# Performance work log

Hardware: AMD Instinct MI355X
Metric: run time of the kernel (lower is better)

## Reference

```python
import jax, jax.numpy as jnp
import numpy as np

E = 1024   # embd_size
H = 16     # heads_num
DH = E // H
DFF = 4 * E
B, T = 2, 2048


def layer_norm(x, g, b, eps=1e-5):
    mu = jnp.mean(x, axis=-1, keepdims=True)
    var = jnp.var(x, axis=-1, keepdims=True)
    return (x - mu) * jax.lax.rsqrt(var + eps) * g + b


def setup_inputs() -> dict:
    key = jax.random.key(0)
    ks = jax.random.split(key, 12)
    s = 0.02
    return {
        "x": jax.random.normal(ks[0], (B, T, E), dtype=jnp.float32),
        "Wq": jax.random.normal(ks[1], (E, E), dtype=jnp.float32) * s,
        "Wk": jax.random.normal(ks[2], (E, E), dtype=jnp.float32) * s,
        "Wv": jax.random.normal(ks[3], (E, E), dtype=jnp.float32) * s,
        "Wo": jax.random.normal(ks[4], (E, E), dtype=jnp.float32) * s,
        "bo": jnp.zeros((E,), dtype=jnp.float32),
        "W1": jax.random.normal(ks[5], (E, DFF), dtype=jnp.float32) * s,
        "b1": jnp.zeros((DFF,), dtype=jnp.float32),
        "W2": jax.random.normal(ks[6], (DFF, E), dtype=jnp.float32) * s,
        "b2": jnp.zeros((E,), dtype=jnp.float32),
        "g1": jnp.ones((E,), dtype=jnp.float32),
        "be1": jnp.zeros((E,), dtype=jnp.float32),
        "g2": jnp.ones((E,), dtype=jnp.float32),
        "be2": jnp.zeros((E,), dtype=jnp.float32),
    }


def reference(x, Wq, Wk, Wv, Wo, bo, W1, b1, W2, b2, g1, be1, g2, be2):
    Bx, Tx, C = x.shape
    # --- self-attention sublayer ---
    h = layer_norm(x, g1, be1)
    # per-head projections; heads concatenated along output dim == stacked weights
    q = (h @ Wq).reshape(Bx, Tx, H, DH)  # [B,T,H,Dh]
    k = (h @ Wk).reshape(Bx, Tx, H, DH)
    v = (h @ Wv).reshape(Bx, Tx, H, DH)
    # NOTE: original scales by full embd_size**-0.5 (C = x.shape[-1]), not head_size
    scale = C ** (-0.5)
    scores = jnp.einsum("bqhd,bkhd->bhqk", q, k) * scale  # [B,H,T,T]
    mask = jnp.tril(jnp.ones((Tx, Tx), dtype=bool))
    scores = jnp.where(mask, scores, -jnp.inf)
    attn = jax.nn.softmax(scores, axis=-1)
    o = jnp.einsum("bhqk,bkhd->bqhd", attn, v).reshape(Bx, Tx, C)
    sa = o @ Wo + bo
    x = x + sa
    # --- feed-forward sublayer ---
    h2 = layer_norm(x, g2, be2)
    ff = jax.nn.relu(h2 @ W1 + b1) @ W2 + b2
    return x + ff
```

## Files before the change

kernel.cpp:

```cpp
#include <hip/hip_runtime.h>
#include <hip/hip_bf16.h>
#include <math.h>

#define Bn 2
#define Tn 2048
#define En 1024
#define Hn 16
#define DFFn 4096
#define Mn (Bn*Tn)
#define QKVLD 3072

typedef __hip_bfloat16 bf16;
typedef unsigned short u16;
typedef unsigned int u32;
typedef __attribute__((ext_vector_type(8))) short short8;
typedef __attribute__((ext_vector_type(4))) float f32x4;

typedef __attribute__((address_space(1))) const void cg_void;
typedef __attribute__((address_space(3))) void lds_void;

#define QSC 0.0450842200278f

#define HBAR() asm volatile("s_waitcnt lgkmcnt(0)\n\ts_barrier" ::: "memory")

__device__ __forceinline__ u16 f2bf(float f) {
    bf16 h = __float2bfloat16(f);
    u16 u; __builtin_memcpy(&u, &h, 2); return u;
}
__device__ __forceinline__ float bf2f(u16 u) {
    u32 x = ((u32)u) << 16; float f; __builtin_memcpy(&f, &x, 4); return f;
}

__global__ __launch_bounds__(256)
void transpose_w4(const float* __restrict__ s0, const float* __restrict__ s1,
                  const float* __restrict__ s2, const float* __restrict__ s3,
                  u16* __restrict__ d0, u16* __restrict__ d1,
                  u16* __restrict__ d2, u16* __restrict__ d3) {
    const float* src = (blockIdx.z == 0) ? s0 : (blockIdx.z == 1) ? s1
                     : (blockIdx.z == 2) ? s2 : s3;
    u16* dst = (blockIdx.z == 0) ? d0 : (blockIdx.z == 1) ? d1
             : (blockIdx.z == 2) ? d2 : d3;
    __shared__ float t[64][65];
    const int r0 = blockIdx.y * 64, c0 = blockIdx.x * 64;
    const int tr = threadIdx.x >> 6, tc = threadIdx.x & 63;
#pragma unroll
    for (int i = 0; i < 16; i++)
        t[tr + i * 4][tc] = src[(size_t)(r0 + tr + i * 4) * 1024 + c0 + tc];
    __syncthreads();
#pragma unroll
    for (int i = 0; i < 16; i++)
        dst[(size_t)(c0 + tr + i * 4) * 1024 + r0 + tc] = f2bf(t[tc][tr + i * 4]);
}

__global__ __launch_bounds__(256)
void transpose_w(const float* __restrict__ src, u16* __restrict__ dst,
                 int R, int C) {
    __shared__ float t[64][65];
    const int r0 = blockIdx.y * 64, c0 = blockIdx.x * 64;
    const int tr = threadIdx.x >> 6, tc = threadIdx.x & 63;
#pragma unroll
    for (int i = 0; i < 16; i++)
        t[tr + i * 4][tc] = src[(size_t)(r0 + tr + i * 4) * C + c0 + tc];
    __syncthreads();
#pragma unroll
    for (int i = 0; i < 16; i++)
        dst[(size_t)(c0 + tr + i * 4) * R + r0 + tc] = f2bf(t[tc][tr + i * 4]);
}

__global__ __launch_bounds__(256)
void vcopy_t(const u16* __restrict__ QKV, u16* __restrict__ Vg) {
    const int bh = blockIdx.z;
    const int t0 = blockIdx.y * 64;
    __shared__ u16 t[64][65];
    const int tr = threadIdx.x >> 6, tc = threadIdx.x & 63;
    const u16* src = QKV + (size_t)(bh >> 4) * 2048 * QKVLD + 2048 + (bh & 15) * 64;
#pragma unroll
    for (int i = 0; i < 16; i++)
        t[tr + i * 4][tc] = src[(size_t)(t0 + tr + i * 4) * QKVLD + tc];
    __syncthreads();
    u16* dst = Vg + (size_t)bh * 64 * 2048;
#pragma unroll
    for (int i = 0; i < 16; i++)
        dst[(size_t)(tr + i * 4) * 2048 + t0 + tc] = t[tc][tr + i * 4];
}

template<typename AT>
__global__ __launch_bounds__(256)
void ln_kernel(const AT* __restrict__ x, const float* __restrict__ g,
               const float* __restrict__ b, u16* __restrict__ out) {
    const int row = blockIdx.x;
    const int tid = threadIdx.x;
    const AT* xp = x + (size_t)row * En;
    float v[4];
    float s = 0.f, sq = 0.f;
#pragma unroll
    for (int i = 0; i < 4; i++) {
        if constexpr (sizeof(AT) == 2) v[i] = bf2f(xp[tid + i * 256]);
        else                           v[i] = (float)xp[tid + i * 256];
        s += v[i];
        sq += v[i] * v[i];
    }
    __shared__ float rs[256], rq[256];
    rs[tid] = s; rq[tid] = sq;
    __syncthreads();
    for (int st = 128; st > 0; st >>= 1) {
        if (tid < st) { rs[tid] += rs[tid + st]; rq[tid] += rq[tid + st]; }
        __syncthreads();
    }
    const float mu  = rs[0] * (1.0f / En);
    const float var = rq[0] * (1.0f / En) - mu * mu;
    const float inv = rsqrtf(var + 1e-5f);
#pragma unroll
    for (int i = 0; i < 4; i++) {
        const int c = tid + i * 256;
        out[(size_t)row * En + c] = f2bf((v[i] - mu) * inv * g[c] + b[c]);
    }
}

__global__ __launch_bounds__(256)
void ff2_init(const u16* __restrict__ X1, const float* __restrict__ b2,
              float* __restrict__ out) {
    const int row = blockIdx.x;
    const int c = threadIdx.x * 4;
    ushort4 a = *(const ushort4*)&X1[(size_t)row * En + c];
    float4 bb = *(const float4*)&b2[c];
    float4 o;
    o.x = bf2f(a.x) + bb.x;
    o.y = bf2f(a.y) + bb.y;
    o.z = bf2f(a.z) + bb.z;
    o.w = bf2f(a.w) + bb.w;
    *(float4*)&out[(size_t)row * En + c] = o;
}

template<int TM, int HAS_BIAS, int RELU, int RES, int OUT_F32, int SCQ,
         int SPLITC, int SPLITA, int ATOM = 0, int XSWZ = 0>
__global__ __launch_bounds__(256)
void gemm_bt(const u16* __restrict__ A, const u16* __restrict__ A2, int ldA,
             const u16* __restrict__ Wt, int ldW,
             const float* __restrict__ bias, const void* __restrict__ res,
             void* __restrict__ Cout, void* __restrict__ Cout2,
             int ldC, int Kd) {
    constexpr int IF = TM / 32;
    __shared__ __align__(16) u16 As[TM * 32];
    __shared__ __align__(16) u16 Bs[128 * 32];
    const int tid  = threadIdx.x;
    const int lane = tid & 63, wv = tid >> 6;
    const int quad = lane >> 4, l16 = lane & 15;

    int bx = blockIdx.x, by = blockIdx.y, bz = blockIdx.z;
    if (XSWZ) {
        const int GX = gridDim.x, GY = gridDim.y;
        const int L = (bz * GY + by) * GX + bx;
        const int xcd = L & 7, slot = L >> 3;
        const int p = slot / GX;
        bx = slot - p * GX;
        const int yz = p * 8 + xcd;
        by = yz & (GY - 1);
        bz = yz >> __builtin_ctz(GY);
    }

    const int m0 = by * TM, n0 = bx * 128;
    const int rw = (wv >> 1) * (TM / 2), cw = (wv & 1) * 64;
    const int lr  = lane >> 2;
    const int gsw = ((lane & 3) ^ ((lane >> 3) & 3)) * 8;
    const int psw = (quad ^ ((l16 >> 1) & 3)) * 8;

    f32x4 acc[IF][4] = {};

    const int kbase = ATOM ? bz * Kd : 0;
    for (int kt = kbase; kt < kbase + Kd; kt += 32) {
        const u16* Ap = (SPLITA && kt >= 2048) ? A2 : A;
        const int  kk = SPLITA ? (kt & 2047) : kt;
        __syncthreads();
#pragma unroll
        for (int t = 0; t < TM / 64; t++) {
            const int row = wv * (TM / 4) + t * 16;
            __builtin_amdgcn_global_load_lds(
                (cg_void*)(const void*)&Ap[(size_t)(m0 + row + lr) * ldA + kk + gsw],
                (lds_void*)(void*)&As[row * 32], 16, 0, 0);
        }
#pragma unroll
        for (int t = 0; t < 2; t++) {
            const int row = wv * 32 + t * 16;
            __builtin_amdgcn_global_load_lds(
                (cg_void*)(const void*)&Wt[(size_t)(n0 + row + lr) * ldW + kt + gsw],
                (lds_void*)(void*)&Bs[row * 32], 16, 0, 0);
        }
        __syncthreads();

        short8 af[IF], bfr[4];
#pragma unroll
        for (int i = 0; i < IF; i++)
            af[i] = *(const short8*)&As[(rw + i * 16 + l16) * 32 + psw];
#pragma unroll
        for (int j = 0; j < 4; j++)
            bfr[j] = *(const short8*)&Bs[(cw + j * 16 + l16) * 32 + psw];
#pragma unroll
        for (int i = 0; i < IF; i++)
#pragma unroll
            for (int j = 0; j < 4; j++)
                acc[i][j] = __builtin_amdgcn_mfma_f32_16x16x32_bf16(
                    af[i], bfr[j], acc[i][j], 0, 0, 0);
    }

    const float qscale = (SCQ && n0 < 1024) ? QSC : 1.0f;
    void* Cp = (SPLITC && n0 >= 2048) ? Cout2 : Cout;
#pragma unroll
    for (int i = 0; i < IF; i++) {
#pragma unroll
        for (int r = 0; r < 4; r++) {
            const int gm = m0 + rw + i * 16 + quad * 4 + r;
#pragma unroll
            for (int j = 0; j < 4; j++) {
                const int gn = n0 + cw + j * 16 + l16;
                const int cn = SPLITC ? (gn & 2047) : gn;
                float c = acc[i][j][r];
                if (HAS_BIAS) c += bias[gn];
                if (RELU) c = fmaxf(c, 0.f);
                if (RES == 1) c += ((const float*)res)[(size_t)gm * ldC + cn];
                if (RES == 2) c += bf2f(((const u16*)res)[(size_t)gm * ldC + cn]);
                if (SCQ) c *= qscale;
                if (ATOM) {
                    atomicAdd(&((float*)Cp)[(size_t)gm * ldC + cn], c);
                } else if (OUT_F32) {
                    ((float*)Cp)[(size_t)gm * ldC + cn] = c;
                } else {
                    ((u16*)Cp)[(size_t)gm * ldC + cn] = f2bf(c);
                }
            }
        }
    }
}

__global__ __launch_bounds__(256)
void flash_pass1(const u16* __restrict__ QKV, const u16* __restrict__ Vg,
                 u16* __restrict__ Op0, u16* __restrict__ Op1qkv,
                 float* __restrict__ stats) {
    const int pr = blockIdx.x >> 1, half = blockIdx.x & 1;
    const int hh = blockIdx.y, bb = blockIdx.z;
    const int tid  = threadIdx.x;
    const int lane = tid & 63, wv = tid >> 6;
    const int quad = lane >> 4, l16 = lane & 15;

    __shared__ __align__(16) u16 Ks[2][64 * 64];
    __shared__ __align__(16) u16 Vt[2][64 * 64];
    __shared__ __align__(16) u16 Ps[4][16 * 64];

    const size_t rowbase = (size_t)(bb * Tn) * QKVLD;
    const u16* Vgh = Vg + (size_t)(bb * Hn + hh) * 64 * 2048;

    const int sr = tid >> 2;
    const int p0 = (tid & 3) | ((sr & 1) << 2);
    const int p1 = p0 ^ 4;
    const int g0 = p0 ^ (sr & 7), g1 = p1 ^ (sr & 7);
    const int lsw = l16 & 7;

    uint4 kA, kB, vA, vB;
    auto prefetch = [&](int kt) {
        const size_t kb = rowbase + (size_t)(kt * 64 + sr) * QKVLD + 1024 + hh * 64;
        kA = *(const uint4*)&QKV[kb + g0 * 8];
        kB = *(const uint4*)&QKV[kb + g1 * 8];
        const size_t vb = (size_t)sr * 2048 + kt * 64;
        vA = *(const uint4*)&Vgh[vb + g0 * 8];
        vB = *(const uint4*)&Vgh[vb + g1 * 8];
    };
    auto writebuf = [&](int buf) {
        *(uint4*)&Ks[buf][sr * 64 + p0 * 8] = kA;
        *(uint4*)&Ks[buf][sr * 64 + p1 * 8] = kB;
        *(uint4*)&Vt[buf][sr * 64 + p0 * 8] = vA;
        *(uint4*)&Vt[buf][sr * 64 + p1 * 8] = vB;
    };

    for (int qsel = 0; qsel < 2; qsel++) {
        const int qt = qsel ? (31 - pr) : pr;
        const int nk = (qt >= half) ? ((qt - half) >> 1) + 1 : 0;
        const int qrow = qt * 64 + wv * 16 + l16;
        const int grow = bb * Tn + qrow;

        f32x4 ot[4] = {};
        float m2 = -INFINITY, lrow = 0.f;

        HBAR();
        if (nk > 0) {
            const u16* qp = QKV + rowbase + (size_t)qrow * QKVLD + hh * 64;
            short8 qf[2];
            qf[0] = *(const short8*)&qp[quad * 8];
            qf[1] = *(const short8*)&qp[32 + quad * 8];

            prefetch(half);
            writebuf(0);
            if (nk > 1) prefetch(half + 2);
            HBAR();

            const bool hasdiag = ((qt ^ half) & 1) == 0;
            for (int f = 0; f < nk; f++) {
                const int cur = f & 1;

                f32x4 st[4] = {};
#pragma unroll
                for (int ks = 0; ks < 2; ks++)
#pragma unroll
                    for (int i = 0; i < 4; i++) {
                        short8 kf = *(const short8*)&Ks[cur][(i * 16 + l16) * 64 +
                                     (((ks * 4 + quad) ^ lsw) * 8)];
                        st[i] = __builtin_amdgcn_mfma_f32_16x16x32_bf16(
                            kf, qf[ks], st[i], 0, 0, 0);
                    }

                float tmax = -INFINITY;
                if (hasdiag && f == nk - 1) {
                    const int qloc = wv * 16 + l16;
#pragma unroll
                    for (int i = 0; i < 4; i++)
#pragma unroll
                        for (int r = 0; r < 4; r++) {
                            float s = st[i][r];
                            if (i * 16 + quad * 4 + r > qloc) s = -INFINITY;
                            st[i][r] = s;
                            tmax = fmaxf(tmax, s);
                        }
                } else {
#pragma unroll
                    for (int i = 0; i < 4; i++)
#pragma unroll
                        for (int r = 0; r < 4; r++)
                            tmax = fmaxf(tmax, st[i][r]);
                }
                tmax = fmaxf(tmax, __shfl_xor(tmax, 16));
                tmax = fmaxf(tmax, __shfl_xor(tmax, 32));

                const float mnew = fmaxf(m2, tmax);
                const float alpha = exp2f(m2 - mnew);
                m2 = mnew;
                float psum = 0.f;
#pragma unroll
                for (int i = 0; i < 4; i++)
#pragma unroll
                    for (int r = 0; r < 4; r++) {
                        const float e = exp2f(st[i][r] - mnew);
                        st[i][r] = e;
                        psum += e;
                    }
                psum += __shfl_xor(psum, 16);
                psum += __shfl_xor(psum, 32);
                lrow = lrow * alpha + psum;
#pragma unroll
                for (int i = 0; i < 4; i++) ot[i] *= alpha;

#pragma unroll
                for (int i = 0; i < 4; i++) {
                    uint2 w;
                    w.x = (u32)f2bf(st[i][0]) | ((u32)f2bf(st[i][1]) << 16);
                    w.y = (u32)f2bf(st[i][2]) | ((u32)f2bf(st[i][3]) << 16);
                    const int g = (i * 2 + (quad >> 1)) ^ lsw;
                    *(uint2*)&Ps[wv][l16 * 64 + g * 8 + (quad & 1) * 4] = w;
                }
                asm volatile("s_waitcnt lgkmcnt(0)" ::: "memory");

#pragma unroll
                for (int ks = 0; ks < 2; ks++) {
                    short8 pf = *(const short8*)&Ps[wv][l16 * 64 +
                                 (((ks * 4 + quad) ^ lsw) * 8)];
#pragma unroll
                    for (int i = 0; i < 4; i++) {
                        short8 vf = *(const short8*)&Vt[cur][(i * 16 + l16) * 64 +
                                     (((ks * 4 + quad) ^ lsw) * 8)];
                        ot[i] = __builtin_amdgcn_mfma_f32_16x16x32_bf16(
                            vf, pf, ot[i], 0, 0, 0);
                    }
                }

                if (f + 1 < nk) {
                    writebuf(cur ^ 1);
                    if (f + 2 < nk) prefetch(half + 2 * (f + 2));
                    HBAR();
                }
            }
        }

        u16* op = (half == 0) ? (Op0 + (size_t)grow * 1024 + hh * 64)
                              : (Op1qkv + (size_t)grow * QKVLD + 2048 + hh * 64);
#pragma unroll
        for (int i = 0; i < 4; i++) {
            ushort4 o4;
            o4.x = f2bf(ot[i][0]); o4.y = f2bf(ot[i][1]);
            o4.z = f2bf(ot[i][2]); o4.w = f2bf(ot[i][3]);
            *(ushort4*)&op[i * 16 + quad * 4] = o4;
        }
        if (quad == 0) {
            stats[((size_t)(half * 2 + 0) * 4096 + grow) * 16 + hh] = m2;
            stats[((size_t)(half * 2 + 1) * 4096 + grow) * 16 + hh] = lrow;
        }
    }
}

__global__ __launch_bounds__(256)
void flash_merge(u16* __restrict__ QKV, const u16* __restrict__ Op0,
                 const float* __restrict__ stats) {
    const int row = blockIdx.x;
    const int tid = threadIdx.x;
    const int col = tid * 4;
    const int hh = col >> 6;
    const float m0 = stats[((size_t)0 * 4096 + row) * 16 + hh];
    const float l0 = stats[((size_t)1 * 4096 + row) * 16 + hh];
    const float m1 = stats[((size_t)2 * 4096 + row) * 16 + hh];
    const float l1 = stats[((size_t)3 * 4096 + row) * 16 + hh];
    const float m  = fmaxf(m0, m1);
    const float w0 = exp2f(m0 - m), w1 = exp2f(m1 - m);
    const float inv = 1.0f / (w0 * l0 + w1 * l1);
    ushort4 a = *(const ushort4*)&Op0[(size_t)row * 1024 + col];
    ushort4 b = *(const ushort4*)&QKV[(size_t)row * QKVLD + 2048 + col];
    ushort4 o;
    o.x = f2bf((w0 * bf2f(a.x) + w1 * bf2f(b.x)) * inv);
    o.y = f2bf((w0 * bf2f(a.y) + w1 * bf2f(b.y)) * inv);
    o.z = f2bf((w0 * bf2f(a.z) + w1 * bf2f(b.z)) * inv);
    o.w = f2bf((w0 * bf2f(a.w) + w1 * bf2f(b.w)) * inv);
    *(ushort4*)&QKV[(size_t)row * QKVLD + col] = o;
}

extern "C" void kernel_launch(void* const* d_in, const int* in_sizes, int n_in,
                              void* d_out, int out_size, void* d_ws, size_t ws_size,
                              hipStream_t stream) {
    const float* x   = (const float*)d_in[0];
    const float* Wq  = (const float*)d_in[1];
    const float* Wk  = (const float*)d_in[2];
    const float* Wv  = (const float*)d_in[3];
    const float* Wo  = (const float*)d_in[4];
    const float* bo  = (const float*)d_in[5];
    const float* W1  = (const float*)d_in[6];
    const float* b1  = (const float*)d_in[7];
    const float* W2  = (const float*)d_in[8];
    const float* b2  = (const float*)d_in[9];
    const float* g1  = (const float*)d_in[10];
    const float* be1 = (const float*)d_in[11];
    const float* g2  = (const float*)d_in[12];
    const float* be2 = (const float*)d_in[13];

    char* wsb = (char*)d_ws;
    u16*   QKV = (u16*)wsb;
    u16*   F1a = (u16*)wsb;
    u16*   W2T = (u16*)(wsb + 16u * 1024 * 1024);
    u16*   Op0 = (u16*)(wsb + 24u * 1024 * 1024);
    u16*   X1b = Op0;
    u16*   Vg  = (u16*)(wsb + 32u * 1024 * 1024);
    u16*   F1b = Vg;
    u16*   h     = (u16*)d_out;
    u16*   WT    = (u16*)((char*)d_out + 8u * 1024 * 1024);
    u16*   WqkvT = WT;
    u16*   WoT   = WT + 3u * 1024 * 1024;
    float* stats = (float*)WT;
    u16*   W1T   = WT;

    transpose_w4<<<dim3(16, 16, 4), 256, 0, stream>>>(
        Wq, Wk, Wv, Wo,
        WqkvT, WqkvT + 1024u * 1024, WqkvT + 2048u * 1024, WoT);

    ln_kernel<float><<<Mn, 256, 0, stream>>>(x, g1, be1, h);

    gemm_bt<128, 0, 0, 0, 0, 1, 0, 0, 0, 1><<<dim3(24, 32), 256, 0, stream>>>(
        h, nullptr, En, WqkvT, En, nullptr, nullptr, QKV, nullptr, QKVLD, En);

    vcopy_t<<<dim3(1, 32, 32), 256, 0, stream>>>(QKV, Vg);

    flash_pass1<<<dim3(32, Hn, Bn), 256, 0, stream>>>(QKV, Vg, Op0, QKV, stats);

    flash_merge<<<Mn, 256, 0, stream>>>(QKV, Op0, stats);

    gemm_bt<64, 1, 0, 1, 0, 0, 0, 0, 0, 1><<<dim3(8, 64), 256, 0, stream>>>(
        QKV, nullptr, QKVLD, WoT, En, bo, x, X1b, nullptr, En, En);

    transpose_w<<<dim3(64, 16), 256, 0, stream>>>(W1, W1T, 1024, 4096);
    transpose_w<<<dim3(16, 64), 256, 0, stream>>>(W2, W2T, 4096, 1024);

    ln_kernel<u16><<<Mn, 256, 0, stream>>>(X1b, g2, be2, h);

    gemm_bt<128, 1, 1, 0, 0, 0, 1, 0, 0, 1><<<dim3(32, 32), 256, 0, stream>>>(
        h, nullptr, En, W1T, En, b1, nullptr, F1a, F1b, 2048, En);

    ff2_init<<<Mn, 256, 0, stream>>>(X1b, b2, (float*)d_out);

    gemm_bt<128, 0, 0, 0, 1, 0, 0, 1, 1, 1><<<dim3(8, 32, 2), 256, 0, stream>>>(
        F1a, F1b, 2048, W2T, DFFn, nullptr, nullptr, (float*)d_out, nullptr,
        En, 2048);
}
```

Measured before the change: 387.7 us.

## Double-buffer GEMM LDS tiles to overlap global loads with MFMA compute

Splits the GEMM k-loop into stage and compute phases over two LDS buffers, so the global-to-LDS loads for the next k-slice are issued before the MFMAs on the current one. It replaces the two barriers per k-step with one vmcnt wait plus barrier per half-step. The cost is doubled LDS footprint, which may lower occupancy. The loop now steps by 64 and always stages kt+32, so it assumes Kd is a multiple of 64.

Result: no change. 392.6 us (+1.3%).

```diff
diff --git a/kernel.cpp b/kernel.cpp
--- a/kernel.cpp
+++ b/kernel.cpp
@@ -22,6 +22,9 @@
 #define QSC 0.0450842200278f
 
 #define HBAR() asm volatile("s_waitcnt lgkmcnt(0)\n\ts_barrier" ::: "memory")
+
+#define GBAR() do { asm volatile("s_waitcnt vmcnt(0)" ::: "memory"); \
+                    __syncthreads(); } while (0)
 
 __device__ __forceinline__ u16 f2bf(float f) {
     bf16 h = __float2bfloat16(f);
@@ -141,8 +144,8 @@
              void* __restrict__ Cout, void* __restrict__ Cout2,
              int ldC, int Kd) {
     constexpr int IF = TM / 32;
-    __shared__ __align__(16) u16 As[TM * 32];
-    __shared__ __align__(16) u16 Bs[128 * 32];
+    __shared__ __align__(16) u16 As[2][TM * 32];
+    __shared__ __align__(16) u16 Bs[2][128 * 32];
     const int tid  = threadIdx.x;
     const int lane = tid & 63, wv = tid >> 6;
     const int quad = lane >> 4, l16 = lane & 15;
@@ -167,40 +170,51 @@
 
     f32x4 acc[IF][4] = {};
 
-    const int kbase = ATOM ? bz * Kd : 0;
-    for (int kt = kbase; kt < kbase + Kd; kt += 32) {
+    auto stage = [&](int buf, int kt) {
         const u16* Ap = (SPLITA && kt >= 2048) ? A2 : A;
         const int  kk = SPLITA ? (kt & 2047) : kt;
-        __syncthreads();
 #pragma unroll
         for (int t = 0; t < TM / 64; t++) {
             const int row = wv * (TM / 4) + t * 16;
             __builtin_amdgcn_global_load_lds(
                 (cg_void*)(const void*)&Ap[(size_t)(m0 + row + lr) * ldA + kk + gsw],
-                (lds_void*)(void*)&As[row * 32], 16, 0, 0);
+                (lds_void*)(void*)&As[buf][row * 32], 16, 0, 0);
         }
 #pragma unroll
         for (int t = 0; t < 2; t++) {
             const int row = wv * 32 + t * 16;
             __builtin_amdgcn_global_load_lds(
                 (cg_void*)(const void*)&Wt[(size_t)(n0 + row + lr) * ldW + kt + gsw],
-                (lds_void*)(void*)&Bs[row * 32], 16, 0, 0);
-        }
-        __syncthreads();
-
+                (lds_void*)(void*)&Bs[buf][row * 32], 16, 0, 0);
+        }
+    };
+    auto compute = [&](int buf) {
         short8 af[IF], bfr[4];
 #pragma unroll
         for (int i = 0; i < IF; i++)
-            af[i] = *(const short8*)&As[(rw + i * 16 + l16) * 32 + psw];
+            af[i] = *(const short8*)&As[buf][(rw + i * 16 + l16) * 32 + psw];
 #pragma unroll
         for (int j = 0; j < 4; j++)
-            bfr[j] = *(const short8*)&Bs[(cw + j * 16 + l16) * 32 + psw];
+            bfr[j] = *(const short8*)&Bs[buf][(cw + j * 16 + l16) * 32 + psw];
 #pragma unroll
         for (int i = 0; i < IF; i++)
 #pragma unroll
             for (int j = 0; j < 4; j++)
                 acc[i][j] = __builtin_amdgcn_mfma_f32_16x16x32_bf16(
                     af[i], bfr[j], acc[i][j], 0, 0, 0);
+    };
+
+    const int kbase = ATOM ? bz * Kd : 0;
+    const int kend  = kbase + Kd;
+    stage(0, kbase);
+    GBAR();
+    for (int kt = kbase; kt < kend; kt += 64) {
+        stage(1, kt + 32);
+        compute(0);
+        GBAR();
+        if (kt + 64 < kend) stage(0, kt + 64);
+        compute(1);
+        GBAR();
     }
 
     const float qscale = (SCQ && n0 < 1024) ? QSC : 1.0f;
```
